# Optimization experiments

Measured on AMD Instinct MI355X. Metric: run time of the kernel, lower is better.

## Reference

```python
import jax, jax.numpy as jnp
from jax import lax
import numpy as np

N_QUBITS = 8


def _apply_1q(state, w, n, m00, m01, m10, m11):
    # state: (B, 2, 2, ..., 2); wire w lives on axis 1+w (wire 0 = most significant)
    st = jnp.moveaxis(state, 1 + w, -1)
    a0, a1 = st[..., 0], st[..., 1]
    b0 = m00 * a0 + m01 * a1
    b1 = m10 * a0 + m11 * a1
    st = jnp.stack([b0, b1], axis=-1)
    return jnp.moveaxis(st, -1, 1 + w)


def _apply_rx(state, theta, w, n):
    # RX(t) = [[cos t/2, -i sin t/2], [-i sin t/2, cos t/2]], per-batch theta
    shp = (-1,) + (1,) * (n - 1)
    c = jnp.cos(theta / 2).reshape(shp).astype(jnp.complex64)
    s = (-1j) * jnp.sin(theta / 2).reshape(shp).astype(jnp.complex64)
    return _apply_1q(state, w, n, c, s, s, c)


def _apply_rz(state, theta, w, n):
    # RZ(t) = diag(e^{-it/2}, e^{+it/2})
    shp = (-1,) + (1,) * (n - 1)
    e = jnp.exp(-0.5j * theta.astype(jnp.complex64)).reshape(shp)
    return _apply_1q(state, w, n, e, jnp.zeros_like(e), jnp.zeros_like(e), jnp.conj(e))


def _apply_cnot(state, ctrl, tgt, n):
    st = jnp.moveaxis(state, (1 + ctrl, 1 + tgt), (-2, -1))
    st = jnp.stack([st[..., 0, :], st[..., 1, ::-1]], axis=-2)
    return jnp.moveaxis(st, (-2, -1), (1 + ctrl, 1 + tgt))


def _circuit_probs(params):
    # params: (B, n). Simulate the fixed PennyLane circuit: for each wire w:
    # RX(params[w]) on w, RZ(params[(w+1)%n]) on w, CNOT(w, (w+1)%n).
    B, n = params.shape
    state = jnp.zeros((B, 2 ** n), jnp.complex64).at[:, 0].set(1.0)
    state = state.reshape((B,) + (2,) * n)
    for w in range(n):
        state = _apply_rx(state, params[:, w], w, n)
        state = _apply_rz(state, params[:, (w + 1) % n], w, n)
        state = _apply_cnot(state, w, (w + 1) % n, n)
    probs = jnp.abs(state.reshape(B, -1)) ** 2  # (B, 2^n), wire 0 most significant
    p = probs[:, :n]
    return p / jnp.sum(p, axis=1, keepdims=True)


def _qgate(W, b, x):
    params = x @ W.T + b  # (B, n_qubits)
    return _circuit_probs(params)


def setup_inputs() -> dict:
    key = jax.random.key(0)
    ks = jax.random.split(key, 9)
    S, B, D, N = 1024, 128, 256, N_QUBITS
    fan_in = D + N
    lim = 1.0 / np.sqrt(fan_in)
    u = lambda k, shape: jax.random.uniform(k, shape, jnp.float32, -lim, lim)
    return {
        "inputs": jax.random.normal(ks[0], (S, B, D), jnp.float32),
        "Wf": u(ks[1], (N, fan_in)), "bf": u(ks[2], (N,)),
        "Wi": u(ks[3], (N, fan_in)), "bi": u(ks[4], (N,)),
        "Wu": u(ks[5], (N, fan_in)), "bu": u(ks[6], (N,)),
        "Wo": u(ks[7], (N, fan_in)), "bo": u(ks[8], (N,)),
    }


def reference(inputs, Wf, bf, Wi, bi, Wu, bu, Wo, bo):
    S, B, D = inputs.shape
    N = Wf.shape[0]  # hidden_dim == n_qubits
    h0 = jnp.zeros((B, N), inputs.dtype)
    c0 = jnp.zeros((B, N), inputs.dtype)

    def step(carry, x):
        h, c = carry
        comb = jnp.concatenate([x, h], axis=1)  # (B, D+N)
        f = _qgate(Wf, bf, comb)
        i = _qgate(Wi, bi, comb)
        g = jnp.tanh(_qgate(Wu, bu, comb))
        o = _qgate(Wo, bo, comb)
        c_new = f * c + i * g
        h_new = o * jnp.tanh(c_new)
        return (h_new, c_new), h_new

    (h_n, c_n), outputs = lax.scan(step, (h0, c0), inputs)
    return outputs, h_n, c_n
```

## Files before the change

### kernel.cpp

```cpp
#include <hip/hip_runtime.h>

#define S_STEPS 1024
#define BATCH 128
#define NQ 8

#define XW_COMPRESSED_FLOATS (BATCH * 20 * 1024)

using v2f     = float __attribute__((ext_vector_type(2)));
using frag_ab = __attribute__((ext_vector_type(8))) short;
using frag_cd = __attribute__((ext_vector_type(4))) float;

#define INV2PI 0.15915494309189535f

template<int CTRL>
__device__ __forceinline__ float dppf(float x) {
  return __int_as_float(__builtin_amdgcn_update_dpp(0, __float_as_int(x), CTRL, 0xf, 0xf, true));
}
__device__ __forceinline__ short f2bf(float f) {
  unsigned u = __float_as_uint(f);
  return (short)((u + 0x7FFFu + ((u >> 16) & 1u)) >> 16);
}
__device__ __forceinline__ float bf2f(short h) {
  return __uint_as_float(((unsigned)(unsigned short)h) << 16);
}

__global__ __launch_bounds__(512) void qlstm_pre(
    const float* __restrict__ x,
    const float* __restrict__ Wf, const float* __restrict__ bf_,
    const float* __restrict__ Wi, const float* __restrict__ bi,
    const float* __restrict__ Wu, const float* __restrict__ bu,
    const float* __restrict__ Wo, const float* __restrict__ bo,
    float* __restrict__ xw)
{
  __shared__ float xbuf[16 * 256];
  __shared__ float red[8 * 520];

  const int tid  = threadIdx.x;
  const int lane = tid & 63;
  const int wid  = tid >> 6;
  const int m    = lane & 15;
  const int kg   = lane >> 4;

  frag_ab awh[2], awl[2];
#pragma unroll
  for (int n = 0; n < 2; ++n) {
    const int c = n * 16 + m;
    const int g = c >> 3, w = c & 7;
    const float* Wg = (g == 0) ? Wf : (g == 1) ? Wi : (g == 2) ? Wu : Wo;
    const float* p = Wg + w * 264 + wid * 32 + kg * 8;
    float4 a  = *(const float4*)(p);
    float4 bq = *(const float4*)(p + 4);
    float vv[8] = {a.x, a.y, a.z, a.w, bq.x, bq.y, bq.z, bq.w};
#pragma unroll
    for (int j = 0; j < 8; ++j) {
      float wv = vv[j] * INV2PI;
      short h = f2bf(wv);
      awh[n][j] = h;
      awl[n][j] = f2bf(wv - bf2f(h));
    }
  }

  const int c  = tid >> 4, mm = tid & 15;
  const int v  = ((c >> 4) << 2) | (c & 3);
  const int lp = (((c >> 2) & 3) << 4) | mm;
  const int gg = c >> 3, ww = c & 7;
  const int widx = (ww==0)?0:(ww==1)?1:(ww==5)?2:(ww==6)?3:(ww==7)?4:-1;
  const float* bg = (gg == 0) ? bf_ : (gg == 1) ? bi : (gg == 2) ? bu : bo;
  const float bias = bg[ww] * INV2PI;

#pragma unroll 1
  for (int it = 0; it < 8; ++it) {
    const int pid = blockIdx.x * 8 + it;
    const int t0i = pid >> 7;
    const int b   = pid & 127;
    const int t0  = t0i << 4;

    {
      const int r = tid >> 5, s = tid & 31;
      const float* xrow = x + ((size_t)(t0 + r) * 128 + b) * 256;
      float4 f0 = *(const float4*)(xrow + s * 4);
      float4 f1 = *(const float4*)(xrow + 128 + s * 4);
      *(float4*)&xbuf[r * 256 + 4 * ((s)      ^ (r & 7))] = f0;
      *(float4*)&xbuf[r * 256 + 4 * ((32 + s) ^ (r & 7))] = f1;
    }
    __syncthreads();

    float4 v0 = *(const float4*)&xbuf[m * 256 + 4 * ((wid * 8 + kg * 2)     ^ (m & 7))];
    float4 v1 = *(const float4*)&xbuf[m * 256 + 4 * ((wid * 8 + kg * 2 + 1) ^ (m & 7))];
    float xf[8] = {v0.x, v0.y, v0.z, v0.w, v1.x, v1.y, v1.z, v1.w};
    frag_ab xh, xl;
#pragma unroll
    for (int j = 0; j < 8; ++j) {
      short h = f2bf(xf[j]);
      xh[j] = h;
      xl[j] = f2bf(xf[j] - bf2f(h));
    }

    frag_cd acc0 = {0.f, 0.f, 0.f, 0.f};
    frag_cd acc1 = {0.f, 0.f, 0.f, 0.f};
    acc0 = __builtin_amdgcn_mfma_f32_16x16x32_bf16(awh[0], xh, acc0, 0, 0, 0);
    acc0 = __builtin_amdgcn_mfma_f32_16x16x32_bf16(awl[0], xh, acc0, 0, 0, 0);
    acc0 = __builtin_amdgcn_mfma_f32_16x16x32_bf16(awh[0], xl, acc0, 0, 0, 0);
    acc1 = __builtin_amdgcn_mfma_f32_16x16x32_bf16(awh[1], xh, acc1, 0, 0, 0);
    acc1 = __builtin_amdgcn_mfma_f32_16x16x32_bf16(awl[1], xh, acc1, 0, 0, 0);
    acc1 = __builtin_amdgcn_mfma_f32_16x16x32_bf16(awh[1], xl, acc1, 0, 0, 0);

#pragma unroll
    for (int rho = 0; rho < 4; ++rho) {
      red[(rho)     * 520 + wid * 64 + lane] = acc0[rho];
      red[(4 + rho) * 520 + wid * 64 + lane] = acc1[rho];
    }
    __syncthreads();

    if (widx >= 0) {
      float sum = 0.f;
#pragma unroll
      for (int w8 = 0; w8 < 8; ++w8)
        sum += red[v * 520 + w8 * 64 + lp];
      xw[((size_t)((b * 4 + gg) * 5 + widx)) * 1024 + t0 + mm] = sum + bias;
    }
  }
}

__global__ __launch_bounds__(64) void qlstm_seq(
    const float* __restrict__ xw,
    const float* __restrict__ Wf, const float* __restrict__ Wi,
    const float* __restrict__ Wu, const float* __restrict__ Wo,
    float* __restrict__ out)
{
  const int lane = threadIdx.x;
  const int r = lane & 15, g = r >> 2, k = r & 3;
  const int b = blockIdx.x * 4 + (lane >> 4);
  const int B6 = (k >> 1) & 1, B7 = k & 1;
  const bool isB7 = (B7 != 0);
  const bool isU  = (g == 2);
  const float s6 = B6 ? -1.f : 1.f,        o6 = B6 ? 1.f : 0.f;
  const float s7 = (B7^B6) ? -1.f : 1.f,   o7 = (B7^B6) ? 1.f : 0.f;
  const int wA = (k == 0) ? 0 : (k == 1) ? 5 : 7;
  const int wB = (k == 0) ? 1 : (k == 1) ? 6 : 7;
  const int widxA = (k == 0) ? 0 : (k == 1) ? 2 : 4;
  const int widxB = (k == 0) ? 1 : (k == 1) ? 3 : 4;
  const bool g0 = (g & 1) != 0;
  const bool g1 = (g & 2) != 0;

  const float* Wg = (g == 0) ? Wf : (g == 1) ? Wi : (g == 2) ? Wu : Wo;
  v2f whA2[4], whB2[4];
#pragma unroll
  for (int j2 = 0; j2 < 4; ++j2) {
    whA2[j2] = (v2f){Wg[wA*264+256+2*j2] * INV2PI, Wg[wA*264+256+2*j2+1] * INV2PI};
    whB2[j2] = (v2f){Wg[wB*264+256+2*j2] * INV2PI, Wg[wB*264+256+2*j2+1] * INV2PI};
  }

  v2f h2[4];
#pragma unroll
  for (int j = 0; j < 4; ++j) h2[j] = (v2f){0.f, 0.f};
  float cA = 0.f, cB = 0.f, hqA = 0.f, hqB = 0.f;

  const float* bxw = xw + (size_t)b * 20480;
  const float4* pA = (const float4*)(bxw + (size_t)(g * 5 + widxA) * 1024);
  const float4* pB = (const float4*)(bxw + (size_t)(g * 5 + widxB) * 1024);
  float4 curA = pA[0], nxtA = pA[1];
  float4 curB = pB[0], nxtB = pB[1];

  const int soff = b * 8 + r;
  float houtS[16];

#pragma unroll 1
  for (int Tb = 0; Tb < S_STEPS; Tb += 16) {
#pragma unroll
    for (int sg = 0; sg < 4; ++sg) {
      int gi = (Tb >> 2) + sg;
      int tp = gi + 2; tp = (tp > 255) ? 255 : tp;
      float4 nnA = pA[tp], nnB = pB[tp];
#pragma unroll
      for (int u = 0; u < 4; ++u) {
        float xa = (u==0)?curA.x:(u==1)?curA.y:(u==2)?curA.z:curA.w;
        float xb = (u==0)?curB.x:(u==1)?curB.y:(u==2)?curB.z:curB.w;
        v2f accA = whA2[0]*h2[0]; accA = whA2[1]*h2[1] + accA;
        accA = whA2[2]*h2[2] + accA; accA = whA2[3]*h2[3] + accA;
        v2f accB = whB2[0]*h2[0]; accB = whB2[1]*h2[1] + accB;
        accB = whB2[2]*h2[2] + accB; accB = whB2[3]*h2[3] + accB;
        float pa = (xa + accA.x) + accA.y;
        float pb = (xb + accB.x) + accB.y;
        float ccA = fmaf(0.5f, __builtin_amdgcn_cosf(pa), 0.5f);
        float ccB = fmaf(0.5f, __builtin_amdgcn_cosf(pb), 0.5f);

        float C0 = dppf<0x00>(ccA), C1 = dppf<0x00>(ccB);
        float C5 = dppf<0x55>(ccA), C6 = dppf<0x55>(ccB);
        float C7 = dppf<0xAA>(ccA);

        float S0v = 1.f - C0, S1v = 1.f - C1;
        float P01 = C0 * C1, Q01 = S0v * S1v;
        float sel01 = isB7 ? Q01 : P01;
        float F7  = fmaf(s7, C7, o7);
        float F6A = fmaf(s6, C6, o6);
        float e7  = sel01 * F7;
        float dA  = C5 * F6A;
        float dB  = (1.f + dA) - (C5 + F6A);
        float d56 = C5 * C6;
        float U0  = fmaf(2.f, d56, 1.f - (C5 + C6));
        float S7v = 1.f - C7;
        float T0  = fmaf(fmaf(2.f, C7, -1.f), U0, S7v);
        float sden = fmaf(P01 - Q01, T0, Q01);

        float NA = e7 * dA, NB = e7 * dB;
        float D2  = sden * sden;
        float NA2 = NA * NA,  NB2 = NB * NB;
        float tA1 = fmaf(15.f, D2, NA2), tA2 = fmaf(5.f, NA2, tA1);
        float tB1 = fmaf(15.f, D2, NB2), tB2 = fmaf(5.f, NB2, tB1);
        float numA = isU ? NA * tA1  : NA;
        float denA = isU ? sden * tA2 : sden;
        float numB = isU ? NB * tB1  : NB;
        float denB = isU ? sden * tB2 : sden;
        float pnA = numA * __builtin_amdgcn_rcpf(denA);
        float pnB = numB * __builtin_amdgcn_rcpf(denB);

        float rMA = dppf<0x140>(pnA);
        float rHA = dppf<0x141>(pnA);
        float r1A = dppf<0x1B>(rHA);
        float r3A = dppf<0x1B>(rMA);
        float r2A = dppf<0x141>(rMA);
        float rMB = dppf<0x140>(pnB);
        float rHB = dppf<0x141>(pnB);
        float r1B = dppf<0x1B>(rHB);
        float r3B = dppf<0x1B>(rMB);
        float r2B = dppf<0x141>(rMB);

        float s32A = g0 ? r3A : r2A;  float s10A = g0 ? r1A : pnA;
        float sv1A = g0 ? pnA : r1A;  float s23A = g0 ? r2A : r3A;
        float fvA = g1 ? s32A : s10A;
        float uvA = g1 ? s10A : s32A;
        float ivA = g1 ? s23A : sv1A;
        float ovA = g1 ? sv1A : s23A;
        float s32B = g0 ? r3B : r2B;  float s10B = g0 ? r1B : pnB;
        float sv1B = g0 ? pnB : r1B;  float s23B = g0 ? r2B : r3B;
        float fvB = g1 ? s32B : s10B;
        float uvB = g1 ? s10B : s32B;
        float ivB = g1 ? s23B : sv1B;
        float ovB = g1 ? sv1B : s23B;

        cA = fmaf(fvA, cA, ivA * uvA);
        float c2A = cA * cA;
        float tnA = c2A + 27.f;
        float tdA = fmaf(9.f, c2A, 27.f);
        float thA = (cA * tnA) * __builtin_amdgcn_rcpf(tdA);
        hqA = ovA * __builtin_amdgcn_fmed3f(thA, -1.f, 1.f);
        cB = fmaf(fvB, cB, ivB * uvB);
        float c2B = cB * cB;
        float tnB = c2B + 27.f;
        float tdB = fmaf(9.f, c2B, 27.f);
        float thB = (cB * tnB) * __builtin_amdgcn_rcpf(tdB);
        hqB = ovB * __builtin_amdgcn_fmed3f(thB, -1.f, 1.f);

        h2[0].x = dppf<0x00>(hqA); h2[0].y = dppf<0x55>(hqA);
        h2[1].x = dppf<0xAA>(hqA); h2[1].y = dppf<0xFF>(hqA);
        h2[2].x = dppf<0x00>(hqB); h2[2].y = dppf<0x55>(hqB);
        h2[3].x = dppf<0xAA>(hqB); h2[3].y = dppf<0xFF>(hqB);

        houtS[sg * 4 + u] = (g == 0) ? hqA : hqB;
      }
      curA = nxtA; nxtA = nnA;
      curB = nxtB; nxtB = nnB;
    }
    if (r < 8) {
      float* op = out + (size_t)Tb * (BATCH * NQ) + soff;
#pragma unroll
      for (int tt = 0; tt < 16; ++tt)
        op[(size_t)tt * (BATCH * NQ)] = houtS[tt];
    }
  }
  if (r < 8) {
    size_t o1 = (size_t)S_STEPS * BATCH * NQ + soff;
    out[o1] = (g == 0) ? hqA : hqB;
    out[o1 + (size_t)BATCH * NQ] = (g == 0) ? cA : cB;
  }
}

extern "C" void kernel_launch(void* const* d_in, const int* in_sizes, int n_in,
                              void* d_out, int out_size, void* d_ws, size_t ws_size,
                              hipStream_t stream) {
  const float* x  = (const float*)d_in[0];
  const float* Wf = (const float*)d_in[1];
  const float* bf = (const float*)d_in[2];
  const float* Wi = (const float*)d_in[3];
  const float* bi = (const float*)d_in[4];
  const float* Wu = (const float*)d_in[5];
  const float* bu = (const float*)d_in[6];
  const float* Wo = (const float*)d_in[7];
  const float* bo = (const float*)d_in[8];
  float* xw  = (float*)d_ws;
  float* out = (float*)d_out;

  qlstm_pre<<<1024, 512, 0, stream>>>(x, Wf, bf, Wi, bi, Wu, bu, Wo, bo, xw);
  qlstm_seq<<<32, 64, 0, stream>>>(xw, Wf, Wi, Wu, Wo, out);
}
```

Measured before the change: 449.8 us.

## Fuse projection and recurrence kernels with per-slice counters to overlap

Merges the input-projection kernel and the sequential recurrence kernel into one launch. The first 32 blocks run the recurrence and spin on per-time-slice atomic counters that the producer blocks increment after writing their projected inputs. The goal is to overlap the serial recurrence with the bulk projection work instead of waiting for the whole projection to finish. The fused kernel adds a memset launch and spin-waits, and it relies on the producer blocks being scheduled while the consumer blocks spin. Consumer blocks also now run at 512 threads, 448 of which exit immediately.

```diff
diff --git a/kernel.cpp b/kernel.cpp
--- a/kernel.cpp
+++ b/kernel.cpp
@@ -5,6 +5,7 @@
 #define NQ 8
 
 #define XW_COMPRESSED_FLOATS (BATCH * 20 * 1024)
+#define CNT_BYTE_OFFSET ((size_t)XW_COMPRESSED_FLOATS * 4)
 
 using v2f     = float __attribute__((ext_vector_type(2)));
 using frag_ab = __attribute__((ext_vector_type(8))) short;
@@ -23,111 +24,125 @@
 __device__ __forceinline__ float bf2f(short h) {
   return __uint_as_float(((unsigned)(unsigned short)h) << 16);
 }
-
-__global__ __launch_bounds__(512) void qlstm_pre(
+__device__ __forceinline__ void st_xw(float* p, float v) {
+  __hip_atomic_store((unsigned*)p, __float_as_uint(v),
+                     __ATOMIC_RELAXED, __HIP_MEMORY_SCOPE_AGENT);
+}
+__device__ __forceinline__ void wait_slice(const unsigned* cnt, int s) {
+  while (__hip_atomic_load(&cnt[s], __ATOMIC_ACQUIRE, __HIP_MEMORY_SCOPE_AGENT) < 16u)
+    __builtin_amdgcn_s_sleep(1);
+}
+
+__global__ __launch_bounds__(512) void qlstm_fused(
     const float* __restrict__ x,
     const float* __restrict__ Wf, const float* __restrict__ bf_,
     const float* __restrict__ Wi, const float* __restrict__ bi,
     const float* __restrict__ Wu, const float* __restrict__ bu,
     const float* __restrict__ Wo, const float* __restrict__ bo,
-    float* __restrict__ xw)
-{
-  __shared__ float xbuf[16 * 256];
-  __shared__ float red[8 * 520];
-
-  const int tid  = threadIdx.x;
-  const int lane = tid & 63;
-  const int wid  = tid >> 6;
-  const int m    = lane & 15;
-  const int kg   = lane >> 4;
-
-  frag_ab awh[2], awl[2];
-#pragma unroll
-  for (int n = 0; n < 2; ++n) {
-    const int c = n * 16 + m;
-    const int g = c >> 3, w = c & 7;
-    const float* Wg = (g == 0) ? Wf : (g == 1) ? Wi : (g == 2) ? Wu : Wo;
-    const float* p = Wg + w * 264 + wid * 32 + kg * 8;
-    float4 a  = *(const float4*)(p);
-    float4 bq = *(const float4*)(p + 4);
-    float vv[8] = {a.x, a.y, a.z, a.w, bq.x, bq.y, bq.z, bq.w};
-#pragma unroll
-    for (int j = 0; j < 8; ++j) {
-      float wv = vv[j] * INV2PI;
-      short h = f2bf(wv);
-      awh[n][j] = h;
-      awl[n][j] = f2bf(wv - bf2f(h));
-    }
-  }
-
-  const int c  = tid >> 4, mm = tid & 15;
-  const int v  = ((c >> 4) << 2) | (c & 3);
-  const int lp = (((c >> 2) & 3) << 4) | mm;
-  const int gg = c >> 3, ww = c & 7;
-  const int widx = (ww==0)?0:(ww==1)?1:(ww==5)?2:(ww==6)?3:(ww==7)?4:-1;
-  const float* bg = (gg == 0) ? bf_ : (gg == 1) ? bi : (gg == 2) ? bu : bo;
-  const float bias = bg[ww] * INV2PI;
-
-#pragma unroll 1
-  for (int it = 0; it < 8; ++it) {
-    const int pid = blockIdx.x * 8 + it;
-    const int t0i = pid >> 7;
-    const int b   = pid & 127;
-    const int t0  = t0i << 4;
-
-    {
-      const int r = tid >> 5, s = tid & 31;
-      const float* xrow = x + ((size_t)(t0 + r) * 128 + b) * 256;
-      float4 f0 = *(const float4*)(xrow + s * 4);
-      float4 f1 = *(const float4*)(xrow + 128 + s * 4);
-      *(float4*)&xbuf[r * 256 + 4 * ((s)      ^ (r & 7))] = f0;
-      *(float4*)&xbuf[r * 256 + 4 * ((32 + s) ^ (r & 7))] = f1;
-    }
-    __syncthreads();
-
-    float4 v0 = *(const float4*)&xbuf[m * 256 + 4 * ((wid * 8 + kg * 2)     ^ (m & 7))];
-    float4 v1 = *(const float4*)&xbuf[m * 256 + 4 * ((wid * 8 + kg * 2 + 1) ^ (m & 7))];
-    float xf[8] = {v0.x, v0.y, v0.z, v0.w, v1.x, v1.y, v1.z, v1.w};
-    frag_ab xh, xl;
-#pragma unroll
-    for (int j = 0; j < 8; ++j) {
-      short h = f2bf(xf[j]);
-      xh[j] = h;
-      xl[j] = f2bf(xf[j] - bf2f(h));
-    }
-
-    frag_cd acc0 = {0.f, 0.f, 0.f, 0.f};
-    frag_cd acc1 = {0.f, 0.f, 0.f, 0.f};
-    acc0 = __builtin_amdgcn_mfma_f32_16x16x32_bf16(awh[0], xh, acc0, 0, 0, 0);
-    acc0 = __builtin_amdgcn_mfma_f32_16x16x32_bf16(awl[0], xh, acc0, 0, 0, 0);
-    acc0 = __builtin_amdgcn_mfma_f32_16x16x32_bf16(awh[0], xl, acc0, 0, 0, 0);
-    acc1 = __builtin_amdgcn_mfma_f32_16x16x32_bf16(awh[1], xh, acc1, 0, 0, 0);
-    acc1 = __builtin_amdgcn_mfma_f32_16x16x32_bf16(awl[1], xh, acc1, 0, 0, 0);
-    acc1 = __builtin_amdgcn_mfma_f32_16x16x32_bf16(awh[1], xl, acc1, 0, 0, 0);
-
-#pragma unroll
-    for (int rho = 0; rho < 4; ++rho) {
-      red[(rho)     * 520 + wid * 64 + lane] = acc0[rho];
-      red[(4 + rho) * 520 + wid * 64 + lane] = acc1[rho];
-    }
-    __syncthreads();
-
-    if (widx >= 0) {
-      float sum = 0.f;
-#pragma unroll
-      for (int w8 = 0; w8 < 8; ++w8)
-        sum += red[v * 520 + w8 * 64 + lp];
-      xw[((size_t)((b * 4 + gg) * 5 + widx)) * 1024 + t0 + mm] = sum + bias;
-    }
-  }
-}
-
-__global__ __launch_bounds__(64) void qlstm_seq(
-    const float* __restrict__ xw,
-    const float* __restrict__ Wf, const float* __restrict__ Wi,
-    const float* __restrict__ Wu, const float* __restrict__ Wo,
+    float* __restrict__ xw, unsigned* __restrict__ cnt,
     float* __restrict__ out)
 {
+  if (blockIdx.x >= 32) {
+    __shared__ float xbuf[16 * 256];
+    __shared__ float red[8 * 520];
+
+    const int tid  = threadIdx.x;
+    const int lane = tid & 63;
+    const int wid  = tid >> 6;
+    const int m    = lane & 15;
+    const int kg   = lane >> 4;
+    const int pb   = blockIdx.x - 32;
+
+    frag_ab awh[2], awl[2];
+#pragma unroll
+    for (int n = 0; n < 2; ++n) {
+      const int c = n * 16 + m;
+      const int g = c >> 3, w = c & 7;
+      const float* Wg = (g == 0) ? Wf : (g == 1) ? Wi : (g == 2) ? Wu : Wo;
+      const float* p = Wg + w * 264 + wid * 32 + kg * 8;
+      float4 a  = *(const float4*)(p);
+      float4 bq = *(const float4*)(p + 4);
+      float vv[8] = {a.x, a.y, a.z, a.w, bq.x, bq.y, bq.z, bq.w};
+#pragma unroll
+      for (int j = 0; j < 8; ++j) {
+        float wv = vv[j] * INV2PI;
+        short h = f2bf(wv);
+        awh[n][j] = h;
+        awl[n][j] = f2bf(wv - bf2f(h));
+      }
+    }
+
+    const int c  = tid >> 4, mm = tid & 15;
+    const int v  = ((c >> 4) << 2) | (c & 3);
+    const int lp = (((c >> 2) & 3) << 4) | mm;
+    const int gg = c >> 3, ww = c & 7;
+    const int widx = (ww==0)?0:(ww==1)?1:(ww==5)?2:(ww==6)?3:(ww==7)?4:-1;
+    const float* bg = (gg == 0) ? bf_ : (gg == 1) ? bi : (gg == 2) ? bu : bo;
+    const float bias = bg[ww] * INV2PI;
+
+#pragma unroll 1
+    for (int it = 0; it < 8; ++it) {
+      const int pid = pb * 8 + it;
+      const int t0i = pid >> 7;
+      const int b   = pid & 127;
+      const int t0  = t0i << 4;
+
+      {
+        const int r = tid >> 5, s = tid & 31;
+        const float* xrow = x + ((size_t)(t0 + r) * 128 + b) * 256;
+        float4 f0 = *(const float4*)(xrow + s * 4);
+        float4 f1 = *(const float4*)(xrow + 128 + s * 4);
+        *(float4*)&xbuf[r * 256 + 4 * ((s)      ^ (r & 7))] = f0;
+        *(float4*)&xbuf[r * 256 + 4 * ((32 + s) ^ (r & 7))] = f1;
+      }
+      __syncthreads();
+
+      float4 v0 = *(const float4*)&xbuf[m * 256 + 4 * ((wid * 8 + kg * 2)     ^ (m & 7))];
+      float4 v1 = *(const float4*)&xbuf[m * 256 + 4 * ((wid * 8 + kg * 2 + 1) ^ (m & 7))];
+      float xf[8] = {v0.x, v0.y, v0.z, v0.w, v1.x, v1.y, v1.z, v1.w};
+      frag_ab xh, xl;
+#pragma unroll
+      for (int j = 0; j < 8; ++j) {
+        short h = f2bf(xf[j]);
+        xh[j] = h;
+        xl[j] = f2bf(xf[j] - bf2f(h));
+      }
+
+      frag_cd acc0 = {0.f, 0.f, 0.f, 0.f};
+      frag_cd acc1 = {0.f, 0.f, 0.f, 0.f};
+      acc0 = __builtin_amdgcn_mfma_f32_16x16x32_bf16(awh[0], xh, acc0, 0, 0, 0);
+      acc0 = __builtin_amdgcn_mfma_f32_16x16x32_bf16(awl[0], xh, acc0, 0, 0, 0);
+      acc0 = __builtin_amdgcn_mfma_f32_16x16x32_bf16(awh[0], xl, acc0, 0, 0, 0);
+      acc1 = __builtin_amdgcn_mfma_f32_16x16x32_bf16(awh[1], xh, acc1, 0, 0, 0);
+      acc1 = __builtin_amdgcn_mfma_f32_16x16x32_bf16(awl[1], xh, acc1, 0, 0, 0);
+      acc1 = __builtin_amdgcn_mfma_f32_16x16x32_bf16(awh[1], xl, acc1, 0, 0, 0);
+
+#pragma unroll
+      for (int rho = 0; rho < 4; ++rho) {
+        red[(rho)     * 520 + wid * 64 + lane] = acc0[rho];
+        red[(4 + rho) * 520 + wid * 64 + lane] = acc1[rho];
+      }
+      __syncthreads();
+
+      if (widx >= 0) {
+        float sum = 0.f;
+#pragma unroll
+        for (int w8 = 0; w8 < 8; ++w8)
+          sum += red[v * 520 + w8 * 64 + lp];
+        st_xw(&xw[((size_t)((b * 4 + gg) * 5 + widx)) * 1024 + t0 + mm],
+              sum + bias);
+      }
+    }
+
+    __syncthreads();
+    if (tid == 0)
+      __hip_atomic_fetch_add(&cnt[pb >> 4], 1u, __ATOMIC_RELEASE,
+                             __HIP_MEMORY_SCOPE_AGENT);
+    return;
+  }
+
+  if (threadIdx.x >= 64) return;
+
   const int lane = threadIdx.x;
   const int r = lane & 15, g = r >> 2, k = r & 3;
   const int b = blockIdx.x * 4 + (lane >> 4);
@@ -159,6 +174,8 @@
   const float* bxw = xw + (size_t)b * 20480;
   const float4* pA = (const float4*)(bxw + (size_t)(g * 5 + widxA) * 1024);
   const float4* pB = (const float4*)(bxw + (size_t)(g * 5 + widxB) * 1024);
+
+  wait_slice(cnt, 0);
   float4 curA = pA[0], nxtA = pA[1];
   float4 curB = pB[0], nxtB = pB[1];
 
@@ -167,13 +184,17 @@
 
 #pragma unroll 1
   for (int Tb = 0; Tb < S_STEPS; Tb += 16) {
+    {
+      int s = (Tb >> 4) + 1; if (s > 63) s = 63;
+      wait_slice(cnt, s);
+    }
 #pragma unroll
     for (int sg = 0; sg < 4; ++sg) {
       int gi = (Tb >> 2) + sg;
       int tp = gi + 2; tp = (tp > 255) ? 255 : tp;
       float4 nnA = pA[tp], nnB = pB[tp];
 #pragma unroll
-      for (int u = 0; u < 4; ++u) {
+    for (int u = 0; u < 4; ++u) {
         float xa = (u==0)?curA.x:(u==1)?curA.y:(u==2)?curA.z:curA.w;
         float xb = (u==0)?curB.x:(u==1)?curB.y:(u==2)?curB.z:curB.w;
         v2f accA = whA2[0]*h2[0]; accA = whA2[1]*h2[1] + accA;
@@ -289,8 +310,10 @@
   const float* Wo = (const float*)d_in[7];
   const float* bo = (const float*)d_in[8];
   float* xw  = (float*)d_ws;
+  unsigned* cnt = (unsigned*)((char*)d_ws + CNT_BYTE_OFFSET);
   float* out = (float*)d_out;
 
-  qlstm_pre<<<1024, 512, 0, stream>>>(x, Wf, bf, Wi, bi, Wu, bu, Wo, bo, xw);
-  qlstm_seq<<<32, 64, 0, stream>>>(xw, Wf, Wi, Wu, Wo, out);
-}
+  hipMemsetAsync(cnt, 0, 64 * sizeof(unsigned), stream);
+  qlstm_fused<<<32 + 1024, 512, 0, stream>>>(x, Wf, bf, Wi, bi, Wu, bu, Wo, bo,
+                                             xw, cnt, out);
+}
```

Measured after the change: 477.0 us. 6.1% more time.
